# Kernel tuning notes

Measured on AMD Instinct MI355X. Metric: run time of the kernel, lower is better.

Reference implementation:

```python
import jax, jax.numpy as jnp
import numpy as np

N = 100_000   # nodes
E = 3_200_000 # edges
K = 3         # num_stacks
T = 4         # num_layers (shared weights)
H = 16        # hidden channels of conv1
EPS = 1e-5    # BatchNorm eps


def setup_inputs() -> dict:
    key = jax.random.key(0)
    ks = jax.random.split(key, 12)
    def glorot(k, shape):
        fan = shape[-2] + shape[-1]
        return jax.random.normal(k, shape, jnp.float32) * (2.0 / fan) ** 0.5
    return {
        "x": jax.random.normal(ks[0], (N, 1), jnp.float32),
        "edge_index": jax.random.randint(ks[1], (2, E), 0, N, jnp.int32),
        "edge_weight": jax.random.uniform(ks[2], (E,), jnp.float32),
        # conv1: in=1, out=16  (init_weight [K,Fin,Fout], shared weight [K,Fout,Fout], root [K,Fin,Fout], bias [K,Fout])
        "conv1_init_w": glorot(ks[3], (K, 1, H)),
        "conv1_w": glorot(ks[4], (K, H, H)),
        "conv1_root_w": glorot(ks[5], (K, 1, H)),
        "conv1_bias": jnp.zeros((K, H), jnp.float32),
        # BatchNorm1d(16) in eval mode: running stats + affine params
        "bn1_gamma": jnp.ones((H,), jnp.float32),
        "bn1_beta": jnp.zeros((H,), jnp.float32),
        "bn1_mean": jnp.zeros((H,), jnp.float32),
        "bn1_var": jnp.ones((H,), jnp.float32),
        # conv2: in=16, out=1, act=None
        "conv2_init_w": glorot(ks[6], (K, H, 1)),
        "conv2_w": glorot(ks[7], (K, 1, 1)),
        "conv2_root_w": glorot(ks[8], (K, H, 1)),
        "conv2_bias": jnp.zeros((K, 1), jnp.float32),
    }


def _gcn_norm(edge_index, edge_weight):
    # ARMAConv uses gcn_norm with add_self_loops=False
    row, col = edge_index[0], edge_index[1]
    deg = jax.ops.segment_sum(edge_weight, col, num_segments=N)
    dis = jnp.where(deg > 0, jax.lax.rsqrt(jnp.maximum(deg, 1e-12)), 0.0)
    norm = dis[row] * edge_weight * dis[col]
    return row, col, norm


def _arma(x, row, col, norm, init_w, w, root_w, bias, act):
    # x: [N, Fin]; out per stack: [K, N, Fout]
    root = jnp.einsum('nf,kfo->kno', x, root_w) + bias[:, None, :]
    out = jnp.einsum('nf,kfo->kno', x, init_w)
    for t in range(T):
        if t > 0:
            out = jnp.einsum('kno,kop->knp', out, w)  # shared weight
        msg = out[:, row, :] * norm[None, :, None]     # [K, E, F] gather + scale
        out = jax.ops.segment_sum(msg.transpose(1, 0, 2), col, num_segments=N)  # [N, K, F]
        out = out.transpose(1, 0, 2) + root            # scatter-add + skip (root)
        if act:
            out = jax.nn.relu(out)
    return out.mean(axis=0)  # mean over stacks -> [N, Fout]


def reference(x, edge_index, edge_weight,
              conv1_init_w, conv1_w, conv1_root_w, conv1_bias,
              bn1_gamma, bn1_beta, bn1_mean, bn1_var,
              conv2_init_w, conv2_w, conv2_root_w, conv2_bias):
    row, col, norm = _gcn_norm(edge_index, edge_weight)
    h = _arma(x, row, col, norm, conv1_init_w, conv1_w, conv1_root_w, conv1_bias, act=True)
    # BatchNorm1d (eval) + ReLU; dropout is identity in eval
    h = (h - bn1_mean) * jax.lax.rsqrt(bn1_var + EPS) * bn1_gamma + bn1_beta
    h = jax.nn.relu(h)
    h = _arma(h, row, col, norm, conv2_init_w, conv2_w, conv2_root_w, conv2_bias, act=False)
    return jax.nn.sigmoid(h)  # [N, 1]
```

## Files before the change

kernel.cpp:

```cpp
#include <hip/hip_runtime.h>
#include <math.h>

#define NN 100000
#define NE 3200000
#define NBUCK 391
#define EPB 4096
#define NBLK 782
#define SB_Q 16
#define BN_EPS 1e-5f

static inline size_t alignup(size_t v) { return (v + 255) & ~size_t(255); }

__device__ inline unsigned short f2bf(float x) {
  unsigned u = __float_as_uint(x);
  u += 0x7FFF + ((u >> 16) & 1);
  return (unsigned short)(u >> 16);
}
__device__ inline float bf2f(unsigned short h) {
  return __uint_as_float((unsigned)h << 16);
}

__global__ void k_hist(const int* __restrict__ col, int* __restrict__ cntm) {
  __shared__ int cnt[NBUCK];
  for (int i = threadIdx.x; i < NBUCK; i += 256) cnt[i] = 0;
  __syncthreads();
  int e0 = blockIdx.x * EPB;
  int nE = min(EPB, NE - e0);
  for (int i = threadIdx.x; i < nE; i += 256) atomicAdd(&cnt[col[e0 + i] >> 8], 1);
  __syncthreads();
  int* dst = cntm + (size_t)blockIdx.x * NBUCK;
  for (int i = threadIdx.x; i < NBUCK; i += 256) dst[i] = cnt[i];
}

__global__ void k_scanb(const int* __restrict__ cntm, int* __restrict__ basem,
                        int* __restrict__ btot) {
  __shared__ int s[NBLK][SB_Q + 1];
  int q0 = blockIdx.x * SB_Q;
  int nq = min(SB_Q, NBUCK - q0);
  int t = threadIdx.x;
  for (int idx = t; idx < NBLK * SB_Q; idx += 256) {
    int i = idx >> 4, j = idx & 15;
    s[i][j] = (j < nq) ? cntm[(size_t)i * NBUCK + q0 + j] : 0;
  }
  __syncthreads();
  int wave = t >> 6, lane = t & 63;
  for (int j = wave; j < SB_Q; j += 4) {
    int carry = 0;
    for (int c = 0; c < (NBLK + 63) / 64; ++c) {
      int i = c * 64 + lane;
      int v = (i < NBLK) ? s[i][j] : 0;
      int x = v;
      #pragma unroll
      for (int d = 1; d < 64; d <<= 1) {
        int tt = __shfl_up(x, d, 64);
        if (lane >= d) x += tt;
      }
      if (i < NBLK) s[i][j] = x - v + carry;
      carry += __shfl(x, 63, 64);
    }
    if (lane == 0 && j < nq) btot[q0 + j] = carry;
  }
  __syncthreads();
  for (int idx = t; idx < NBLK * SB_Q; idx += 256) {
    int i = idx >> 4, j = idx & 15;
    if (j < nq) basem[(size_t)i * NBUCK + q0 + j] = s[i][j];
  }
}

__global__ void k_scanq(const int* __restrict__ btot, int* __restrict__ gbase) {
  __shared__ int s[NBUCK];
  __shared__ int c[256];
  const int NCH = (NBUCK + 3) / 4;
  int t = threadIdx.x;
  for (int i = t; i < NBUCK; i += 256) s[i] = btot[i];
  __syncthreads();
  if (t < NCH) {
    int b0 = 4 * t, sum = 0;
    #pragma unroll
    for (int j = 0; j < 4; ++j) if (b0 + j < NBUCK) sum += s[b0 + j];
    c[t] = sum;
  }
  __syncthreads();
  for (int d = 1; d < NCH; d <<= 1) {
    int v = (t < NCH && t >= d) ? c[t - d] : 0;
    __syncthreads();
    if (t < NCH) c[t] += v;
    __syncthreads();
  }
  if (t < NCH) {
    int b0 = 4 * t;
    int run = (t > 0) ? c[t - 1] : 0;
    #pragma unroll
    for (int j = 0; j < 4; ++j)
      if (b0 + j < NBUCK) { int v = s[b0 + j]; s[b0 + j] = run; run += v; }
  }
  __syncthreads();
  for (int i = t; i < NBUCK; i += 256) gbase[i] = s[i];
}

__global__ void k_scat(const int* __restrict__ row, const int* __restrict__ col,
                       const float* __restrict__ ew, const int* __restrict__ basem,
                       const int* __restrict__ gbase, int2* __restrict__ bin) {
  __shared__ int segB[NBUCK];
  __shared__ int cnt[NBUCK];
  __shared__ int csc[256];
  __shared__ int2 stage[EPB];
  __shared__ unsigned short qarr[EPB];
  int b = blockIdx.x, t = threadIdx.x;
  for (int i = t; i < NBUCK; i += 256) {
    segB[i] = gbase[i] + basem[(size_t)b * NBUCK + i];
    cnt[i] = 0;
  }
  __syncthreads();
  int e0 = b * EPB;
  int nE = min(EPB, NE - e0);
  for (int i = t; i < nE; i += 256) atomicAdd(&cnt[col[e0 + i] >> 8], 1);
  __syncthreads();
  const int NCH = (NBUCK + 3) / 4;
  int q4 = 4 * t;
  if (t < NCH) {
    int sum = 0;
    #pragma unroll
    for (int j = 0; j < 4; ++j) if (q4 + j < NBUCK) sum += cnt[q4 + j];
    csc[t] = sum;
  }
  __syncthreads();
  for (int d = 1; d < NCH; d <<= 1) {
    int v = (t < NCH && t >= d) ? csc[t - d] : 0;
    __syncthreads();
    if (t < NCH) csc[t] += v;
    __syncthreads();
  }
  if (t < NCH) {
    int run = (t > 0) ? csc[t - 1] : 0;
    #pragma unroll
    for (int j = 0; j < 4; ++j)
      if (q4 + j < NBUCK) {
        int v = cnt[q4 + j];
        segB[q4 + j] -= run;
        cnt[q4 + j] = run;
        run += v;
      }
  }
  __syncthreads();
  for (int i = t; i < nE; i += 256) {
    int e = e0 + i;
    int cc = col[e], q = cc >> 8;
    int p = atomicAdd(&cnt[q], 1);
    stage[p] = make_int2(row[e] | ((cc & 255) << 17), __float_as_int(ew[e]));
    qarr[p] = (unsigned short)q;
  }
  __syncthreads();
  for (int p = t; p < nE; p += 256) {
    int q = qarr[p];
    bin[segB[q] + p] = stage[p];
  }
}

__global__ void k_build(const int* __restrict__ gbase, const int* __restrict__ btot,
                        const int2* __restrict__ bin,
                        int* __restrict__ csr, float* __restrict__ dis,
                        int* __restrict__ nstart, int* __restrict__ ncnt) {
  __shared__ int cnt[256];
  __shared__ float degw[256];
  __shared__ int off[257];
  int b = blockIdx.x;
  int gb0 = gbase[b];
  int nb = btot[b];
  const int2* gb = bin + gb0;
  for (int i = threadIdx.x; i < 256; i += 256) { cnt[i] = 0; degw[i] = 0.f; }
  __syncthreads();
  for (int i = threadIdx.x; i < nb; i += 256) {
    int2 v = gb[i];
    int c = (v.x >> 17) & 255;
    atomicAdd(&cnt[c], 1);
    atomicAdd(&degw[c], __int_as_float(v.y));
  }
  __syncthreads();
  if (threadIdx.x == 0) {
    int s = 0;
    for (int c = 0; c < 256; ++c) { off[c] = s; s += cnt[c]; }
    off[256] = s;
  }
  __syncthreads();
  for (int c = threadIdx.x; c < 256; c += 256) {
    int n = b * 256 + c;
    if (n < NN) {
      nstart[n] = gb0 + off[c];
      ncnt[n] = cnt[c];
      float d = degw[c];
      dis[n] = (d > 0.f) ? rsqrtf(fmaxf(d, 1e-12f)) : 0.f;
    }
  }
  __syncthreads();
  for (int i = threadIdx.x; i < 256; i += 256) cnt[i] = 0;
  __syncthreads();
  int* cb = csr + gb0;
  for (int i = threadIdx.x; i < nb; i += 256) {
    int2 v = gb[i];
    int c = (v.x >> 17) & 255;
    int pos = off[c] + atomicAdd(&cnt[c], 1);
    float w = __int_as_float(v.y);
    int q = (int)fminf(fmaf(w, 32767.f, 0.5f), 32767.f);
    cb[pos] = (v.x & 0x1FFFF) | (q << 17);
  }
}

__global__ void k_init1(const float* __restrict__ x, const float* __restrict__ rw,
                        const float* __restrict__ bias, const float* __restrict__ dis,
                        float* __restrict__ root1, float* __restrict__ s) {
  int idx = blockIdx.x * 256 + threadIdx.x;
  if (idx >= NN * 16) return;
  int n = idx >> 4, f = idx & 15;
  float xv = x[n];
  if (f == 0) s[n] = dis[n] * xv;
  root1[n * 48 + f]      = xv * rw[f]      + bias[f];
  root1[n * 48 + 16 + f] = xv * rw[16 + f] + bias[16 + f];
  root1[n * 48 + 32 + f] = xv * rw[32 + f] + bias[32 + f];
}

__global__ void k_prop_first(const float* __restrict__ s, const float* __restrict__ root,
                             ushort4* __restrict__ outp, const int* __restrict__ csr,
                             const int* __restrict__ nstart, const int* __restrict__ ncnt,
                             const float* __restrict__ dis, const float* __restrict__ w,
                             const float* __restrict__ iw) {
  __shared__ float ws[768];
  for (int i = threadIdx.x; i < 768; i += 256) ws[i] = w[i];
  __syncthreads();
  int f = threadIdx.x & 15;
  int n = (blockIdx.x * 256 + threadIdx.x) >> 4;
  if (n >= NN) return;
  int e0 = nstart[n], cnt = ncnt[n];
  float g = 0.f;
  for (int i = f; i < cnt; i += 16) {
    int e = csr[e0 + i];
    float we = (float)((unsigned)e >> 17) * (1.f / 32767.f);
    g = fmaf(we, s[e & 0x1FFFF], g);
  }
  #pragma unroll
  for (int d = 8; d; d >>= 1) g += __shfl_xor(g, d, 16);
  float dn = dis[n];
  float dg = dn * g;
  float a0 = fmaxf(fmaf(dg, iw[f],      root[n * 48 + f]),      0.f);
  float a1 = fmaxf(fmaf(dg, iw[16 + f], root[n * 48 + 16 + f]), 0.f);
  float a2 = fmaxf(fmaf(dg, iw[32 + f], root[n * 48 + 32 + f]), 0.f);
  float n0 = 0.f, n1 = 0.f, n2 = 0.f;
  #pragma unroll
  for (int f2 = 0; f2 < 16; ++f2) {
    float b0 = __shfl(a0, f2, 16);
    float b1 = __shfl(a1, f2, 16);
    float b2v = __shfl(a2, f2, 16);
    n0 = fmaf(b0, ws[f2 * 16 + f], n0);
    n1 = fmaf(b1, ws[256 + f2 * 16 + f], n1);
    n2 = fmaf(b2v, ws[512 + f2 * 16 + f], n2);
  }
  ushort4 pk;
  pk.x = f2bf(dn * n0); pk.y = f2bf(dn * n1); pk.z = f2bf(dn * n2); pk.w = 0;
  outp[(size_t)n * 16 + f] = pk;
}

template <bool APPLY_W>
__global__ void k_prop16(const ushort4* __restrict__ in, const float* __restrict__ root,
                         ushort4* __restrict__ outp, const int* __restrict__ csr,
                         const int* __restrict__ nstart, const int* __restrict__ ncnt,
                         const float* __restrict__ dis, const float* __restrict__ w,
                         const float* __restrict__ bng, const float* __restrict__ bnb,
                         const float* __restrict__ bnm, const float* __restrict__ bnv,
                         const float* __restrict__ iw2, const float* __restrict__ rw2,
                         const float* __restrict__ b2,
                         float4* __restrict__ root2, float4* __restrict__ o2) {
  __shared__ float ws[768];
  if (APPLY_W) {
    for (int i = threadIdx.x; i < 768; i += 256) ws[i] = w[i];
    __syncthreads();
  }
  int f = threadIdx.x & 15;
  int n = (blockIdx.x * 256 + threadIdx.x) >> 4;
  if (n >= NN) return;
  int e0 = nstart[n], cnt = ncnt[n];
  float a0 = 0.f, a1 = 0.f, a2 = 0.f;
  int i = 0;
  for (; i + 8 <= cnt; i += 8) {
    int e[8];
    ushort4 v[8];
    #pragma unroll
    for (int j = 0; j < 8; ++j) e[j] = csr[e0 + i + j];
    #pragma unroll
    for (int j = 0; j < 8; ++j) v[j] = in[(size_t)(e[j] & 0x1FFFF) * 16 + f];
    #pragma unroll
    for (int j = 0; j < 8; ++j) {
      float we = (float)((unsigned)e[j] >> 17) * (1.f / 32767.f);
      a0 = fmaf(we, bf2f(v[j].x), a0);
      a1 = fmaf(we, bf2f(v[j].y), a1);
      a2 = fmaf(we, bf2f(v[j].z), a2);
    }
  }
  for (; i + 4 <= cnt; i += 4) {
    int e[4];
    ushort4 v[4];
    #pragma unroll
    for (int j = 0; j < 4; ++j) e[j] = csr[e0 + i + j];
    #pragma unroll
    for (int j = 0; j < 4; ++j) v[j] = in[(size_t)(e[j] & 0x1FFFF) * 16 + f];
    #pragma unroll
    for (int j = 0; j < 4; ++j) {
      float we = (float)((unsigned)e[j] >> 17) * (1.f / 32767.f);
      a0 = fmaf(we, bf2f(v[j].x), a0);
      a1 = fmaf(we, bf2f(v[j].y), a1);
      a2 = fmaf(we, bf2f(v[j].z), a2);
    }
  }
  for (; i < cnt; ++i) {
    int e = csr[e0 + i];
    float we = (float)((unsigned)e >> 17) * (1.f / 32767.f);
    ushort4 v = in[(size_t)(e & 0x1FFFF) * 16 + f];
    a0 = fmaf(we, bf2f(v.x), a0);
    a1 = fmaf(we, bf2f(v.y), a1);
    a2 = fmaf(we, bf2f(v.z), a2);
  }
  float dn = dis[n];
  a0 = fmaxf(fmaf(dn, a0, root[n * 48 + f]), 0.f);
  a1 = fmaxf(fmaf(dn, a1, root[n * 48 + 16 + f]), 0.f);
  a2 = fmaxf(fmaf(dn, a2, root[n * 48 + 32 + f]), 0.f);
  if (APPLY_W) {
    float n0 = 0.f, n1 = 0.f, n2 = 0.f;
    #pragma unroll
    for (int f2 = 0; f2 < 16; ++f2) {
      float b0 = __shfl(a0, f2, 16);
      float b1 = __shfl(a1, f2, 16);
      float b2v = __shfl(a2, f2, 16);
      n0 = fmaf(b0, ws[f2 * 16 + f], n0);
      n1 = fmaf(b1, ws[256 + f2 * 16 + f], n1);
      n2 = fmaf(b2v, ws[512 + f2 * 16 + f], n2);
    }
    ushort4 pk;
    pk.x = f2bf(dn * n0); pk.y = f2bf(dn * n1); pk.z = f2bf(dn * n2); pk.w = 0;
    outp[(size_t)n * 16 + f] = pk;
  } else {
    float mean = (a0 + a1 + a2) * (1.f / 3.f);
    float hv = fmaxf((mean - bnm[f]) * rsqrtf(bnv[f] + BN_EPS) * bng[f] + bnb[f], 0.f);
    float d0 = hv * iw2[f],      r0 = hv * rw2[f];
    float d1 = hv * iw2[16 + f], r1 = hv * rw2[16 + f];
    float d2 = hv * iw2[32 + f], r2 = hv * rw2[32 + f];
    #pragma unroll
    for (int d = 8; d; d >>= 1) {
      d0 += __shfl_xor(d0, d, 16); r0 += __shfl_xor(r0, d, 16);
      d1 += __shfl_xor(d1, d, 16); r1 += __shfl_xor(r1, d, 16);
      d2 += __shfl_xor(d2, d, 16); r2 += __shfl_xor(r2, d, 16);
    }
    if (f == 0) {
      float4 rt, oo;
      rt.x = r0 + b2[0]; rt.y = r1 + b2[1]; rt.z = r2 + b2[2]; rt.w = 0.f;
      oo.x = dn * d0; oo.y = dn * d1; oo.z = dn * d2; oo.w = 0.f;
      root2[n] = rt;
      o2[n] = oo;
    }
  }
}

template <bool LAST>
__global__ void k_prop1(const float4* __restrict__ in, const float4* __restrict__ root,
                        float4* __restrict__ outp, float* __restrict__ outf,
                        const int* __restrict__ csr,
                        const int* __restrict__ nstart, const int* __restrict__ ncnt,
                        const float* __restrict__ dis, const float* __restrict__ w2) {
  int lane = threadIdx.x & 15;
  int n = (blockIdx.x * 256 + threadIdx.x) >> 4;
  if (n >= NN) return;
  int e0 = nstart[n], cnt = ncnt[n];
  float a0 = 0.f, a1 = 0.f, a2 = 0.f;
  for (int i = lane; i < cnt; i += 16) {
    int e = csr[e0 + i];
    float we = (float)((unsigned)e >> 17) * (1.f / 32767.f);
    float4 src = in[e & 0x1FFFF];
    a0 = fmaf(we, src.x, a0);
    a1 = fmaf(we, src.y, a1);
    a2 = fmaf(we, src.z, a2);
  }
  #pragma unroll
  for (int d = 8; d; d >>= 1) {
    a0 += __shfl_xor(a0, d, 16);
    a1 += __shfl_xor(a1, d, 16);
    a2 += __shfl_xor(a2, d, 16);
  }
  if (lane == 0) {
    float dn = dis[n];
    float4 rt = root[n];
    if (LAST) {
      float s = fmaf(dn, a0, rt.x) + fmaf(dn, a1, rt.y) + fmaf(dn, a2, rt.z);
      s *= (1.f / 3.f);
      outf[n] = 1.f / (1.f + expf(-s));
    } else {
      float4 oo;
      oo.x = dn * fmaf(dn, a0, rt.x) * w2[0];
      oo.y = dn * fmaf(dn, a1, rt.y) * w2[1];
      oo.z = dn * fmaf(dn, a2, rt.z) * w2[2];
      oo.w = 0.f;
      outp[n] = oo;
    }
  }
}

extern "C" void kernel_launch(void* const* d_in, const int* in_sizes, int n_in,
                              void* d_out, int out_size, void* d_ws, size_t ws_size,
                              hipStream_t stream) {
  const float* x     = (const float*)d_in[0];
  const int*   ei    = (const int*)d_in[1];
  const float* ew    = (const float*)d_in[2];
  const float* c1_iw = (const float*)d_in[3];
  const float* c1_w  = (const float*)d_in[4];
  const float* c1_rw = (const float*)d_in[5];
  const float* c1_b  = (const float*)d_in[6];
  const float* bn_g  = (const float*)d_in[7];
  const float* bn_b  = (const float*)d_in[8];
  const float* bn_m  = (const float*)d_in[9];
  const float* bn_v  = (const float*)d_in[10];
  const float* c2_iw = (const float*)d_in[11];
  const float* c2_w  = (const float*)d_in[12];
  const float* c2_rw = (const float*)d_in[13];
  const float* c2_b  = (const float*)d_in[14];
  float* out = (float*)d_out;

  char* p = (char*)d_ws;
  auto take = [&](size_t bytes) -> char* { char* r = p; p += alignup(bytes); return r; };
  int*     cntm   = (int*)take((size_t)NBLK * NBUCK * 4);
  int*     basem  = (int*)take((size_t)NBLK * NBUCK * 4);
  int*     btot   = (int*)take((size_t)NBUCK * 4);
  int*     gbase  = (int*)take((size_t)NBUCK * 4);
  int2*    bin    = (int2*)take((size_t)NE * 8);
  int*     csr    = (int*)take((size_t)NE * 4);
  float*   dis    = (float*)take((size_t)NN * 4);
  int*     nst    = (int*)take((size_t)NN * 4);
  int*     ncn    = (int*)take((size_t)NN * 4);
  float*   root1  = (float*)take((size_t)NN * 48 * 4);
  float*   sbuf   = (float*)take((size_t)NN * 4);
  ushort4* bufA   = (ushort4*)take((size_t)NN * 16 * 8);
  ushort4* bufB   = (ushort4*)take((size_t)NN * 16 * 8);
  float4*  root2  = (float4*)take((size_t)NN * 16);
  float4*  o2A    = (float4*)take((size_t)NN * 16);
  float4*  o2B    = (float4*)take((size_t)NN * 16);

  const int* row = ei;
  const int* col = ei + NE;

  const int gP = (NN * 16 + 255) / 256;
  const int gSB = (NBUCK + SB_Q - 1) / SB_Q;

  k_hist <<<NBLK, 256, 0, stream>>>(col, cntm);
  k_scanb<<<gSB, 256, 0, stream>>>(cntm, basem, btot);
  k_scanq<<<1, 256, 0, stream>>>(btot, gbase);
  k_scat <<<NBLK, 256, 0, stream>>>(row, col, ew, basem, gbase, bin);
  k_build<<<NBUCK, 256, 0, stream>>>(gbase, btot, bin, csr, dis, nst, ncn);

  k_init1<<<gP, 256, 0, stream>>>(x, c1_rw, c1_b, dis, root1, sbuf);
  k_prop_first<<<gP, 256, 0, stream>>>(sbuf, root1, bufA, csr, nst, ncn, dis, c1_w, c1_iw);
  k_prop16<true ><<<gP, 256, 0, stream>>>(bufA, root1, bufB, csr, nst, ncn, dis, c1_w,
      nullptr, nullptr, nullptr, nullptr, nullptr, nullptr, nullptr, nullptr, nullptr);
  k_prop16<true ><<<gP, 256, 0, stream>>>(bufB, root1, bufA, csr, nst, ncn, dis, c1_w,
      nullptr, nullptr, nullptr, nullptr, nullptr, nullptr, nullptr, nullptr, nullptr);
  k_prop16<false><<<gP, 256, 0, stream>>>(bufA, root1, nullptr, csr, nst, ncn, dis, nullptr,
      bn_g, bn_b, bn_m, bn_v, c2_iw, c2_rw, c2_b, root2, o2A);

  k_prop1<false><<<gP, 256, 0, stream>>>(o2A, root2, o2B, nullptr, csr, nst, ncn, dis, c2_w);
  k_prop1<false><<<gP, 256, 0, stream>>>(o2B, root2, o2A, nullptr, csr, nst, ncn, dis, c2_w);
  k_prop1<false><<<gP, 256, 0, stream>>>(o2A, root2, o2B, nullptr, csr, nst, ncn, dis, c2_w);
  k_prop1<true ><<<gP, 256, 0, stream>>>(o2B, root2, nullptr, out, csr, nst, ncn, dis, c2_w);
}
```

Before: 398.6 us.

## Use finer buckets, stage bins in LDS, bf16-style edge weights, fuse conv2 passes cooperatively

Node buckets shrink from 256 to 128 nodes, and the CSR build now stages bucket edges in shared memory so the global bin is read only once. Edge weights are packed as truncated-mantissa floats in the top bits, so decoding is a mask instead of an int-to-float convert and multiply. The four conv2 propagation kernels are merged into one cooperative persistent kernel with grid syncs between passes. Risks include lower weight precision, since the rounding changes from 15-bit fixed point to an 8-bit mantissa, dependence on a 1024-block cooperative launch being co-resident, and any buckets larger than SCAP falling back to global memory.

```diff
diff --git a/kernel.cpp b/kernel.cpp
--- a/kernel.cpp
+++ b/kernel.cpp
@@ -1,12 +1,14 @@
 #include <hip/hip_runtime.h>
+#include <hip/hip_cooperative_groups.h>
 #include <math.h>
 
 #define NN 100000
 #define NE 3200000
-#define NBUCK 391
+#define NBUCK 782
 #define EPB 4096
 #define NBLK 782
 #define SB_Q 16
+#define SCAP 4608
 #define BN_EPS 1e-5f
 
 static inline size_t alignup(size_t v) { return (v + 255) & ~size_t(255); }
@@ -19,6 +21,9 @@
 __device__ inline float bf2f(unsigned short h) {
   return __uint_as_float((unsigned)h << 16);
 }
+__device__ inline float edgew(int e) {
+  return __uint_as_float((unsigned)e & 0xFFFE0000u);
+}
 
 __global__ void k_hist(const int* __restrict__ col, int* __restrict__ cntm) {
   __shared__ int cnt[NBUCK];
@@ -26,7 +31,7 @@
   __syncthreads();
   int e0 = blockIdx.x * EPB;
   int nE = min(EPB, NE - e0);
-  for (int i = threadIdx.x; i < nE; i += 256) atomicAdd(&cnt[col[e0 + i] >> 8], 1);
+  for (int i = threadIdx.x; i < nE; i += 256) atomicAdd(&cnt[col[e0 + i] >> 7], 1);
   __syncthreads();
   int* dst = cntm + (size_t)blockIdx.x * NBUCK;
   for (int i = threadIdx.x; i < NBUCK; i += 256) dst[i] = cnt[i];
@@ -114,7 +119,7 @@
   __syncthreads();
   int e0 = b * EPB;
   int nE = min(EPB, NE - e0);
-  for (int i = t; i < nE; i += 256) atomicAdd(&cnt[col[e0 + i] >> 8], 1);
+  for (int i = t; i < nE; i += 256) atomicAdd(&cnt[col[e0 + i] >> 7], 1);
   __syncthreads();
   const int NCH = (NBUCK + 3) / 4;
   int q4 = 4 * t;
@@ -145,9 +150,9 @@
   __syncthreads();
   for (int i = t; i < nE; i += 256) {
     int e = e0 + i;
-    int cc = col[e], q = cc >> 8;
+    int cc = col[e], q = cc >> 7;
     int p = atomicAdd(&cnt[q], 1);
-    stage[p] = make_int2(row[e] | ((cc & 255) << 17), __float_as_int(ew[e]));
+    stage[p] = make_int2(row[e] | ((cc & 127) << 17), __float_as_int(ew[e]));
     qarr[p] = (unsigned short)q;
   }
   __syncthreads();
@@ -161,30 +166,32 @@
                         const int2* __restrict__ bin,
                         int* __restrict__ csr, float* __restrict__ dis,
                         int* __restrict__ nstart, int* __restrict__ ncnt) {
-  __shared__ int cnt[256];
-  __shared__ float degw[256];
-  __shared__ int off[257];
+  __shared__ int2 stage[SCAP];
+  __shared__ int cnt[128];
+  __shared__ float degw[128];
+  __shared__ int off[129];
   int b = blockIdx.x;
   int gb0 = gbase[b];
   int nb = btot[b];
   const int2* gb = bin + gb0;
-  for (int i = threadIdx.x; i < 256; i += 256) { cnt[i] = 0; degw[i] = 0.f; }
+  for (int i = threadIdx.x; i < 128; i += 256) { cnt[i] = 0; degw[i] = 0.f; }
   __syncthreads();
   for (int i = threadIdx.x; i < nb; i += 256) {
     int2 v = gb[i];
-    int c = (v.x >> 17) & 255;
+    if (i < SCAP) stage[i] = v;
+    int c = (v.x >> 17) & 127;
     atomicAdd(&cnt[c], 1);
     atomicAdd(&degw[c], __int_as_float(v.y));
   }
   __syncthreads();
   if (threadIdx.x == 0) {
     int s = 0;
-    for (int c = 0; c < 256; ++c) { off[c] = s; s += cnt[c]; }
-    off[256] = s;
-  }
-  __syncthreads();
-  for (int c = threadIdx.x; c < 256; c += 256) {
-    int n = b * 256 + c;
+    for (int c = 0; c < 128; ++c) { off[c] = s; s += cnt[c]; }
+    off[128] = s;
+  }
+  __syncthreads();
+  for (int c = threadIdx.x; c < 128; c += 256) {
+    int n = b * 128 + c;
     if (n < NN) {
       nstart[n] = gb0 + off[c];
       ncnt[n] = cnt[c];
@@ -193,16 +200,16 @@
     }
   }
   __syncthreads();
-  for (int i = threadIdx.x; i < 256; i += 256) cnt[i] = 0;
+  for (int i = threadIdx.x; i < 128; i += 256) cnt[i] = 0;
   __syncthreads();
   int* cb = csr + gb0;
   for (int i = threadIdx.x; i < nb; i += 256) {
-    int2 v = gb[i];
-    int c = (v.x >> 17) & 255;
+    int2 v = (i < SCAP) ? stage[i] : gb[i];
+    int c = (v.x >> 17) & 127;
     int pos = off[c] + atomicAdd(&cnt[c], 1);
-    float w = __int_as_float(v.y);
-    int q = (int)fminf(fmaf(w, 32767.f, 0.5f), 32767.f);
-    cb[pos] = (v.x & 0x1FFFF) | (q << 17);
+    unsigned u = (unsigned)v.y;
+    u += 0xFFFFu + ((u >> 17) & 1);
+    cb[pos] = (v.x & 0x1FFFF) | (int)(u & 0xFFFE0000u);
   }
 }
 
@@ -234,8 +241,7 @@
   float g = 0.f;
   for (int i = f; i < cnt; i += 16) {
     int e = csr[e0 + i];
-    float we = (float)((unsigned)e >> 17) * (1.f / 32767.f);
-    g = fmaf(we, s[e & 0x1FFFF], g);
+    g = fmaf(edgew(e), s[e & 0x1FFFF], g);
   }
   #pragma unroll
   for (int d = 8; d; d >>= 1) g += __shfl_xor(g, d, 16);
@@ -289,7 +295,7 @@
     for (int j = 0; j < 8; ++j) v[j] = in[(size_t)(e[j] & 0x1FFFF) * 16 + f];
     #pragma unroll
     for (int j = 0; j < 8; ++j) {
-      float we = (float)((unsigned)e[j] >> 17) * (1.f / 32767.f);
+      float we = edgew(e[j]);
       a0 = fmaf(we, bf2f(v[j].x), a0);
       a1 = fmaf(we, bf2f(v[j].y), a1);
       a2 = fmaf(we, bf2f(v[j].z), a2);
@@ -304,7 +310,7 @@
     for (int j = 0; j < 4; ++j) v[j] = in[(size_t)(e[j] & 0x1FFFF) * 16 + f];
     #pragma unroll
     for (int j = 0; j < 4; ++j) {
-      float we = (float)((unsigned)e[j] >> 17) * (1.f / 32767.f);
+      float we = edgew(e[j]);
       a0 = fmaf(we, bf2f(v[j].x), a0);
       a1 = fmaf(we, bf2f(v[j].y), a1);
       a2 = fmaf(we, bf2f(v[j].z), a2);
@@ -312,7 +318,7 @@
   }
   for (; i < cnt; ++i) {
     int e = csr[e0 + i];
-    float we = (float)((unsigned)e >> 17) * (1.f / 32767.f);
+    float we = edgew(e);
     ushort4 v = in[(size_t)(e & 0x1FFFF) * 16 + f];
     a0 = fmaf(we, bf2f(v.x), a0);
     a1 = fmaf(we, bf2f(v.y), a1);
@@ -358,45 +364,58 @@
   }
 }
 
-template <bool LAST>
-__global__ void k_prop1(const float4* __restrict__ in, const float4* __restrict__ root,
-                        float4* __restrict__ outp, float* __restrict__ outf,
-                        const int* __restrict__ csr,
-                        const int* __restrict__ nstart, const int* __restrict__ ncnt,
-                        const float* __restrict__ dis, const float* __restrict__ w2) {
+__global__ __launch_bounds__(256)
+void k_conv2_all(const float4* __restrict__ o2A, float4* __restrict__ o2B,
+                 const float4* __restrict__ root2, float* __restrict__ outf,
+                 const int* __restrict__ csr, const int* __restrict__ nstart,
+                 const int* __restrict__ ncnt, const float* __restrict__ dis,
+                 const float* __restrict__ w2) {
+  cooperative_groups::grid_group grid = cooperative_groups::this_grid();
   int lane = threadIdx.x & 15;
-  int n = (blockIdx.x * 256 + threadIdx.x) >> 4;
-  if (n >= NN) return;
-  int e0 = nstart[n], cnt = ncnt[n];
-  float a0 = 0.f, a1 = 0.f, a2 = 0.f;
-  for (int i = lane; i < cnt; i += 16) {
-    int e = csr[e0 + i];
-    float we = (float)((unsigned)e >> 17) * (1.f / 32767.f);
-    float4 src = in[e & 0x1FFFF];
-    a0 = fmaf(we, src.x, a0);
-    a1 = fmaf(we, src.y, a1);
-    a2 = fmaf(we, src.z, a2);
-  }
-  #pragma unroll
-  for (int d = 8; d; d >>= 1) {
-    a0 += __shfl_xor(a0, d, 16);
-    a1 += __shfl_xor(a1, d, 16);
-    a2 += __shfl_xor(a2, d, 16);
-  }
-  if (lane == 0) {
-    float dn = dis[n];
-    float4 rt = root[n];
-    if (LAST) {
-      float s = fmaf(dn, a0, rt.x) + fmaf(dn, a1, rt.y) + fmaf(dn, a2, rt.z);
-      s *= (1.f / 3.f);
-      outf[n] = 1.f / (1.f + expf(-s));
-    } else {
-      float4 oo;
-      oo.x = dn * fmaf(dn, a0, rt.x) * w2[0];
-      oo.y = dn * fmaf(dn, a1, rt.y) * w2[1];
-      oo.z = dn * fmaf(dn, a2, rt.z) * w2[2];
-      oo.w = 0.f;
-      outp[n] = oo;
+  int gid0 = (int)((blockIdx.x * 256 + threadIdx.x) >> 4);
+  int gstr = (int)((gridDim.x * 256) >> 4);
+  float w0 = w2[0], w1 = w2[1], w2v = w2[2];
+  for (int pass = 0; pass < 4; ++pass) {
+    const float4* in = (pass & 1) ? (const float4*)o2B : o2A;
+    float4* outp = (pass & 1) ? (float4*)o2A : o2B;
+    bool last = (pass == 3);
+    for (int n = gid0; n < NN; n += gstr) {
+      int e0 = nstart[n], cnt = ncnt[n];
+      float a0 = 0.f, a1 = 0.f, a2 = 0.f;
+      for (int i = lane; i < cnt; i += 16) {
+        int e = csr[e0 + i];
+        float we = edgew(e);
+        float4 src = in[e & 0x1FFFF];
+        a0 = fmaf(we, src.x, a0);
+        a1 = fmaf(we, src.y, a1);
+        a2 = fmaf(we, src.z, a2);
+      }
+      #pragma unroll
+      for (int d = 8; d; d >>= 1) {
+        a0 += __shfl_xor(a0, d, 16);
+        a1 += __shfl_xor(a1, d, 16);
+        a2 += __shfl_xor(a2, d, 16);
+      }
+      if (lane == 0) {
+        float dn = dis[n];
+        float4 rt = root2[n];
+        if (last) {
+          float s = fmaf(dn, a0, rt.x) + fmaf(dn, a1, rt.y) + fmaf(dn, a2, rt.z);
+          s *= (1.f / 3.f);
+          outf[n] = 1.f / (1.f + expf(-s));
+        } else {
+          float4 oo;
+          oo.x = dn * fmaf(dn, a0, rt.x) * w0;
+          oo.y = dn * fmaf(dn, a1, rt.y) * w1;
+          oo.z = dn * fmaf(dn, a2, rt.z) * w2v;
+          oo.w = 0.f;
+          outp[n] = oo;
+        }
+      }
+    }
+    if (pass < 3) {
+      __threadfence();
+      grid.sync();
     }
   }
 }
@@ -461,8 +480,8 @@
   k_prop16<false><<<gP, 256, 0, stream>>>(bufA, root1, nullptr, csr, nst, ncn, dis, nullptr,
       bn_g, bn_b, bn_m, bn_v, c2_iw, c2_rw, c2_b, root2, o2A);
 
-  k_prop1<false><<<gP, 256, 0, stream>>>(o2A, root2, o2B, nullptr, csr, nst, ncn, dis, c2_w);
-  k_prop1<false><<<gP, 256, 0, stream>>>(o2B, root2, o2A, nullptr, csr, nst, ncn, dis, c2_w);
-  k_prop1<false><<<gP, 256, 0, stream>>>(o2A, root2, o2B, nullptr, csr, nst, ncn, dis, c2_w);
-  k_prop1<true ><<<gP, 256, 0, stream>>>(o2B, root2, nullptr, out, csr, nst, ncn, dis, c2_w);
-}
+  void* args[] = {(void*)&o2A, (void*)&o2B, (void*)&root2, (void*)&out,
+                  (void*)&csr, (void*)&nst, (void*)&ncn, (void*)&dis, (void*)&c2_w};
+  hipLaunchCooperativeKernel((const void*)k_conv2_all, dim3(1024), dim3(256),
+                             args, 0, stream);
+}
```

After: 1.045 ms. +162.3%, slower.
